# Kernel tuning notes

Hardware: AMD Instinct MI355X
Metric: run time of the kernel (lower is better)

## Reference

```python
import jax, jax.numpy as jnp
import numpy as np

N_INPUT = 2
N_NODES = 4
C = 64          # channel width of every state
B, H, W = 64, 32, 32
N_EDGES = sum(N_INPUT + i for i in range(N_NODES))  # 2+3+4+5 = 14


def conv1x1(x, w):
    # x: [B,C,H,W], w: [C_out,C_in] -> [B,C_out,H,W]
    return jnp.einsum('bchw,oc->bohw', x, w)


def setup_inputs() -> dict:
    key = jax.random.key(0)
    k0, k1, k2, k3 = jax.random.split(key, 4)
    x0 = jax.random.normal(k0, (B, C, H, W), dtype=jnp.float32)
    x1 = jax.random.normal(k1, (B, C, H, W), dtype=jnp.float32)
    # preproc: one 1x1 conv per input state
    W_pre = jax.random.normal(k2, (N_INPUT, C, C), dtype=jnp.float32) * (1.0 / np.sqrt(C))
    # one 1x1 conv per DAG edge (flattened in enumeration order)
    W_edge = jax.random.normal(k3, (N_EDGES, C, C), dtype=jnp.float32) * (1.0 / np.sqrt(C))
    return {'x0': x0, 'x1': x1, 'W_pre': W_pre, 'W_edge': W_edge}


def reference(x0, x1, W_pre, W_edge):
    # preprocess inputs -> initial states
    states = [conv1x1(x0, W_pre[0]), conv1x1(x1, W_pre[1])]
    e = 0
    for i in range(N_NODES):
        n_states = N_INPUT + i
        # gather every prior state, apply edge op (ReLU -> 1x1 conv), sum-merge
        s_cur = conv1x1(jax.nn.relu(states[0]), W_edge[e])
        for s in range(1, n_states):
            s_cur = s_cur + conv1x1(jax.nn.relu(states[s]), W_edge[e + s])
        e += n_states
        states.append(s_cur)
    # merger_out: concat intermediate node states (start=n_input) on channels
    return jnp.concatenate(states[N_INPUT:], axis=1)  # [B, N_NODES*C, H, W]
```

## Files before the change

### kernel.cpp

```cpp
#include <hip/hip_runtime.h>


typedef _Float16 f16;
typedef _Float16 f16x8 __attribute__((ext_vector_type(8)));
typedef float    f32x4 __attribute__((ext_vector_type(4)));

#define RSH 72
#define SB  (64 * RSH)

__device__ __forceinline__ unsigned int pkrtz(float a, float b) {
    __fp16 h2 __attribute__((ext_vector_type(2))) = __builtin_amdgcn_cvt_pkrtz(a, b);
    return __builtin_bit_cast(unsigned int, h2);
}

__global__ __launch_bounds__(256) void wconv_kernel(
    const float* __restrict__ Wpre, const float* __restrict__ Wedge,
    f16* __restrict__ ws)
{
    const int u   = blockIdx.x * 256 + threadIdx.x;
    const int k   = u >> 9;
    const int rem = u & 511;
    const int g   = rem >> 6;
    const int row = rem & 63;
    const float* src = ((k < 2) ? (Wpre + k * 4096) : (Wedge + (k - 2) * 4096))
                       + row * 64 + (g >> 2) * 32 + (g & 3) * 8;
    float4 v0 = ((const float4*)src)[0];
    float4 v1 = ((const float4*)src)[1];
    ((uint4*)ws)[u] = make_uint4(pkrtz(v0.x, v0.y), pkrtz(v0.z, v0.w),
                                 pkrtz(v1.x, v1.y), pkrtz(v1.z, v1.w));
}

__global__ __launch_bounds__(128, 2) void dag_kernel(
    const float* __restrict__ x0, const float* __restrict__ x1,
    const f16* __restrict__ wf, float* __restrict__ out)
{
    __shared__ __align__(16) f16 lds[4 * SB];

    const int t    = threadIdx.x;
    const int lane = t & 63;
    const int wv   = t >> 6;
    const int pl   = lane & 15;
    const int q    = lane >> 4;

    const int blk = blockIdx.x;
    const int b   = blk >> 4;
    const int hw0 = (blk & 15) * 64;

    const float* xg[2] = { x0 + b * 65536 + hw0, x1 + b * 65536 + hw0 };
    float* outg = out + b * 262144 + hw0;

    const f16* wl = wf + q * 512 + pl * 8;

    f16x8 wA[2][2][4];
    #pragma unroll
    for (int kb = 0; kb < 2; ++kb)
        #pragma unroll
        for (int i = 0; i < 4; ++i)
            wA[0][kb][i] = *(const f16x8*)(wl + kb * 2048 + i * 128);

    {
        const int p = t & 63, h = t >> 6;
        #pragma unroll
        for (int inp = 0; inp < 2; ++inp) {
            const float* src = xg[inp] + (h * 32) * 1024 + p;
            unsigned int u[16];
            #pragma unroll
            for (int i = 0; i < 16; ++i)
                u[i] = pkrtz(src[(2 * i) * 1024], src[(2 * i + 1) * 1024]);
            uint4* dst = (uint4*)(lds + (2 + inp) * SB + p * RSH + h * 32);
            dst[0] = make_uint4(u[0],  u[1],  u[2],  u[3]);
            dst[1] = make_uint4(u[4],  u[5],  u[6],  u[7]);
            dst[2] = make_uint4(u[8],  u[9],  u[10], u[11]);
            dst[3] = make_uint4(u[12], u[13], u[14], u[15]);
        }
    }
    __syncthreads();

    f32x4 accA[2][4] = {};
    f32x4 accB[2][4] = {};

    const int widx_tab[16] = {0,1, 2,3, 4,5,6, 7,11, 8,12, 9,13, 14, 10, 15};
    const int src_tab [16] = {2,3, 0,1, 0,1,2, 0,0,  1,1,  2,2,  3,  3,  0};
    const int asel_tab[16] = {0,0, 0,0, 0,0,0, 0,1,  0,1,  0,1,  1,  0,  1};
    const int out_tab [16] = {-1,-1, -1,0, -1,-1,1, -1,-1, -1,-1, -1,-1, -1, 2, 3};
    const int dst_tab [16] = { 0, 1, -1,2, -1,-1,3, -1,-1, -1,-1, -1,-1, -1, 0,-1};

    #pragma unroll
    for (int k = 0; k < 16; ++k) {
        const int cur = k & 1, nxt = cur ^ 1;

        if (k < 15) {
            const f16* wn = wl + widx_tab[k + 1] * 4096;
            #pragma unroll
            for (int kb = 0; kb < 2; ++kb)
                #pragma unroll
                for (int i = 0; i < 4; ++i)
                    wA[nxt][kb][i] = *(const f16x8*)(wn + kb * 2048 + i * 128);
        }

        const f16* S = lds + src_tab[k] * SB;
        f16x8 bf[2][2];
        #pragma unroll
        for (int jj = 0; jj < 2; ++jj)
            #pragma unroll
            for (int kb = 0; kb < 2; ++kb)
                bf[jj][kb] = *(const f16x8*)(S + (wv * 32 + jj * 16 + pl) * RSH
                                               + kb * 32 + q * 8);

        auto step = [&](f32x4 (&acc)[2][4]) {
            #pragma unroll
            for (int jj = 0; jj < 2; ++jj)
                #pragma unroll
                for (int kb = 0; kb < 2; ++kb)
                    #pragma unroll
                    for (int i = 0; i < 4; ++i)
                        acc[jj][i] = __builtin_amdgcn_mfma_f32_16x16x32_f16(
                                         wA[cur][kb][i], bf[jj][kb], acc[jj][i], 0, 0, 0);
        };
        auto retire = [&](f32x4 (&acc)[2][4]) {
            if (out_tab[k] >= 0) {
                #pragma unroll
                for (int jj = 0; jj < 2; ++jj) {
                    const int p = wv * 32 + jj * 16 + pl;
                    #pragma unroll
                    for (int i = 0; i < 4; ++i) {
                        const int c = i * 16 + q * 4;
                        #pragma unroll
                        for (int r = 0; r < 4; ++r)
                            outg[(out_tab[k] * 64 + c + r) * 1024 + p] = acc[jj][i][r];
                    }
                }
            }
            if (dst_tab[k] >= 0) {
                f16* D = lds + dst_tab[k] * SB;
                #pragma unroll
                for (int jj = 0; jj < 2; ++jj) {
                    f16* Dp = D + (wv * 32 + jj * 16 + pl) * RSH;
                    #pragma unroll
                    for (int i = 0; i < 4; ++i) {
                        unsigned int u0 = pkrtz(fmaxf(acc[jj][i][0], 0.f),
                                                fmaxf(acc[jj][i][1], 0.f));
                        unsigned int u1 = pkrtz(fmaxf(acc[jj][i][2], 0.f),
                                                fmaxf(acc[jj][i][3], 0.f));
                        *(uint2*)(Dp + i * 16 + q * 4) = make_uint2(u0, u1);
                    }
                }
            }
            if (out_tab[k] >= 0 || dst_tab[k] >= 0) {
                #pragma unroll
                for (int jj = 0; jj < 2; ++jj)
                    #pragma unroll
                    for (int i = 0; i < 4; ++i)
                        acc[jj][i] = (f32x4){0.f, 0.f, 0.f, 0.f};
            }
        };

        if (asel_tab[k] == 0) { step(accA); retire(accA); }
        else                  { step(accB); retire(accB); }
    }
}

extern "C" void kernel_launch(void* const* d_in, const int* in_sizes, int n_in,
                              void* d_out, int out_size, void* d_ws, size_t ws_size,
                              hipStream_t stream) {
    const float* x0    = (const float*)d_in[0];
    const float* x1    = (const float*)d_in[1];
    const float* Wpre  = (const float*)d_in[2];
    const float* Wedge = (const float*)d_in[3];
    float* outp        = (float*)d_out;
    f16*   wfrag       = (f16*)d_ws;

    wconv_kernel<<<dim3(32), dim3(256), 0, stream>>>(Wpre, Wedge, wfrag);
    dag_kernel<<<dim3(1024), dim3(128), 0, stream>>>(x0, x1, wfrag, outp);
}
```

Before: 104.3 us.

## Swap MFMA operands for DAG edges to vectorize output stores; triple-buffer weights

```diff
diff --git a/kernel.cpp b/kernel.cpp
--- a/kernel.cpp
+++ b/kernel.cpp
@@ -49,14 +49,23 @@
     const float* xg[2] = { x0 + b * 65536 + hw0, x1 + b * 65536 + hw0 };
     float* outg = out + b * 262144 + hw0;
 
+    const int widx_tab[16] = {0,1, 2,3, 4,5,6, 7,11, 8,12, 9,13, 14, 10, 15};
+    const int src_tab [16] = {2,3, 0,1, 0,1,2, 0,0,  1,1,  2,2,  3,  3,  0};
+    const int asel_tab[16] = {0,0, 0,0, 0,0,0, 0,1,  0,1,  0,1,  1,  0,  1};
+    const int out_tab [16] = {-1,-1, -1,0, -1,-1,1, -1,-1, -1,-1, -1,-1, -1, 2, 3};
+    const int dst_tab [16] = { 0, 1, -1,2, -1,-1,3, -1,-1, -1,-1, -1,-1, -1, 0,-1};
+
     const f16* wl = wf + q * 512 + pl * 8;
 
-    f16x8 wA[2][2][4];
+    f16x8 wA[3][2][4];
     #pragma unroll
-    for (int kb = 0; kb < 2; ++kb)
+    for (int s = 0; s < 2; ++s)
         #pragma unroll
-        for (int i = 0; i < 4; ++i)
-            wA[0][kb][i] = *(const f16x8*)(wl + kb * 2048 + i * 128);
+        for (int kb = 0; kb < 2; ++kb)
+            #pragma unroll
+            for (int i = 0; i < 4; ++i)
+                wA[s][kb][i] = *(const f16x8*)(wl + widx_tab[s] * 4096
+                                               + kb * 2048 + i * 128);
 
     {
         const int p = t & 63, h = t >> 6;
@@ -79,23 +88,18 @@
     f32x4 accA[2][4] = {};
     f32x4 accB[2][4] = {};
 
-    const int widx_tab[16] = {0,1, 2,3, 4,5,6, 7,11, 8,12, 9,13, 14, 10, 15};
-    const int src_tab [16] = {2,3, 0,1, 0,1,2, 0,0,  1,1,  2,2,  3,  3,  0};
-    const int asel_tab[16] = {0,0, 0,0, 0,0,0, 0,1,  0,1,  0,1,  1,  0,  1};
-    const int out_tab [16] = {-1,-1, -1,0, -1,-1,1, -1,-1, -1,-1, -1,-1, -1, 2, 3};
-    const int dst_tab [16] = { 0, 1, -1,2, -1,-1,3, -1,-1, -1,-1, -1,-1, -1, 0,-1};
-
     #pragma unroll
     for (int k = 0; k < 16; ++k) {
-        const int cur = k & 1, nxt = cur ^ 1;
+        const int cur = k % 3;
 
-        if (k < 15) {
-            const f16* wn = wl + widx_tab[k + 1] * 4096;
+        if (k < 14) {
+            const f16* wn = wl + widx_tab[k + 2] * 4096;
+            const int s = (k + 2) % 3;
             #pragma unroll
             for (int kb = 0; kb < 2; ++kb)
                 #pragma unroll
                 for (int i = 0; i < 4; ++i)
-                    wA[nxt][kb][i] = *(const f16x8*)(wn + kb * 2048 + i * 128);
+                    wA[s][kb][i] = *(const f16x8*)(wn + kb * 2048 + i * 128);
         }
 
         const f16* S = lds + src_tab[k] * SB;
@@ -107,6 +111,8 @@
                 bf[jj][kb] = *(const f16x8*)(S + (wv * 32 + jj * 16 + pl) * RSH
                                                + kb * 32 + q * 8);
 
+        const bool swp = (k >= 2);
+
         auto step = [&](f32x4 (&acc)[2][4]) {
             #pragma unroll
             for (int jj = 0; jj < 2; ++jj)
@@ -114,35 +120,48 @@
                 for (int kb = 0; kb < 2; ++kb)
                     #pragma unroll
                     for (int i = 0; i < 4; ++i)
-                        acc[jj][i] = __builtin_amdgcn_mfma_f32_16x16x32_f16(
-                                         wA[cur][kb][i], bf[jj][kb], acc[jj][i], 0, 0, 0);
+                        acc[jj][i] = swp
+                            ? __builtin_amdgcn_mfma_f32_16x16x32_f16(
+                                  bf[jj][kb], wA[cur][kb][i], acc[jj][i], 0, 0, 0)
+                            : __builtin_amdgcn_mfma_f32_16x16x32_f16(
+                                  wA[cur][kb][i], bf[jj][kb], acc[jj][i], 0, 0, 0);
         };
         auto retire = [&](f32x4 (&acc)[2][4]) {
             if (out_tab[k] >= 0) {
                 #pragma unroll
                 for (int jj = 0; jj < 2; ++jj) {
-                    const int p = wv * 32 + jj * 16 + pl;
+                    const int p0 = wv * 32 + jj * 16 + q * 4;
                     #pragma unroll
-                    for (int i = 0; i < 4; ++i) {
-                        const int c = i * 16 + q * 4;
-                        #pragma unroll
-                        for (int r = 0; r < 4; ++r)
-                            outg[(out_tab[k] * 64 + c + r) * 1024 + p] = acc[jj][i][r];
-                    }
+                    for (int i = 0; i < 4; ++i)
+                        *(f32x4*)(outg + (out_tab[k] * 64 + i * 16 + pl) * 1024
+                                       + p0) = acc[jj][i];
                 }
             }
             if (dst_tab[k] >= 0) {
                 f16* D = lds + dst_tab[k] * SB;
-                #pragma unroll
-                for (int jj = 0; jj < 2; ++jj) {
-                    f16* Dp = D + (wv * 32 + jj * 16 + pl) * RSH;
+                if (!swp) {
                     #pragma unroll
-                    for (int i = 0; i < 4; ++i) {
-                        unsigned int u0 = pkrtz(fmaxf(acc[jj][i][0], 0.f),
-                                                fmaxf(acc[jj][i][1], 0.f));
-                        unsigned int u1 = pkrtz(fmaxf(acc[jj][i][2], 0.f),
-                                                fmaxf(acc[jj][i][3], 0.f));
-                        *(uint2*)(Dp + i * 16 + q * 4) = make_uint2(u0, u1);
+                    for (int jj = 0; jj < 2; ++jj) {
+                        f16* Dp = D + (wv * 32 + jj * 16 + pl) * RSH;
+                        #pragma unroll
+                        for (int i = 0; i < 4; ++i) {
+                            unsigned int u0 = pkrtz(fmaxf(acc[jj][i][0], 0.f),
+                                                    fmaxf(acc[jj][i][1], 0.f));
+                            unsigned int u1 = pkrtz(fmaxf(acc[jj][i][2], 0.f),
+                                                    fmaxf(acc[jj][i][3], 0.f));
+                            *(uint2*)(Dp + i * 16 + q * 4) = make_uint2(u0, u1);
+                        }
+                    }
+                } else {
+                    #pragma unroll
+                    for (int jj = 0; jj < 2; ++jj) {
+                        const int p0 = wv * 32 + jj * 16 + q * 4;
+                        #pragma unroll
+                        for (int i = 0; i < 4; ++i)
+                            #pragma unroll
+                            for (int r = 0; r < 4; ++r)
+                                D[(p0 + r) * RSH + i * 16 + pl] =
+                                    (f16)fmaxf(acc[jj][i][r], 0.f);
                     }
                 }
             }
```

Result: slower. 107.2 us (+2.8%).

## Split output channels across four waves and swap MFMA operands for vectorized stores

Applied to the files above, without the earlier changes.

```diff
diff --git a/kernel.cpp b/kernel.cpp
--- a/kernel.cpp
+++ b/kernel.cpp
@@ -30,7 +30,7 @@
                                  pkrtz(v1.x, v1.y), pkrtz(v1.z, v1.w));
 }
 
-__global__ __launch_bounds__(128, 2) void dag_kernel(
+__global__ __launch_bounds__(256, 4) void dag_kernel(
     const float* __restrict__ x0, const float* __restrict__ x1,
     const f16* __restrict__ wf, float* __restrict__ out)
 {
@@ -38,7 +38,7 @@
 
     const int t    = threadIdx.x;
     const int lane = t & 63;
-    const int wv   = t >> 6;
+    const int w    = t >> 6;
     const int pl   = lane & 15;
     const int q    = lane >> 4;
 
@@ -49,41 +49,37 @@
     const float* xg[2] = { x0 + b * 65536 + hw0, x1 + b * 65536 + hw0 };
     float* outg = out + b * 262144 + hw0;
 
-    const f16* wl = wf + q * 512 + pl * 8;
+    const f16* wl = wf + q * 512 + (w * 16 + pl) * 8;
 
-    f16x8 wA[2][2][4];
+    f16x8 wA[2][2];
     #pragma unroll
     for (int kb = 0; kb < 2; ++kb)
-        #pragma unroll
-        for (int i = 0; i < 4; ++i)
-            wA[0][kb][i] = *(const f16x8*)(wl + kb * 2048 + i * 128);
+        wA[0][kb] = *(const f16x8*)(wl + kb * 2048);
 
     {
         const int p = t & 63, h = t >> 6;
         #pragma unroll
         for (int inp = 0; inp < 2; ++inp) {
-            const float* src = xg[inp] + (h * 32) * 1024 + p;
-            unsigned int u[16];
+            const float* src = xg[inp] + (h * 16) * 1024 + p;
+            unsigned int u[8];
             #pragma unroll
-            for (int i = 0; i < 16; ++i)
+            for (int i = 0; i < 8; ++i)
                 u[i] = pkrtz(src[(2 * i) * 1024], src[(2 * i + 1) * 1024]);
-            uint4* dst = (uint4*)(lds + (2 + inp) * SB + p * RSH + h * 32);
-            dst[0] = make_uint4(u[0],  u[1],  u[2],  u[3]);
-            dst[1] = make_uint4(u[4],  u[5],  u[6],  u[7]);
-            dst[2] = make_uint4(u[8],  u[9],  u[10], u[11]);
-            dst[3] = make_uint4(u[12], u[13], u[14], u[15]);
+            uint4* dst = (uint4*)(lds + (2 + inp) * SB + p * RSH + h * 16);
+            dst[0] = make_uint4(u[0], u[1], u[2], u[3]);
+            dst[1] = make_uint4(u[4], u[5], u[6], u[7]);
         }
     }
     __syncthreads();
 
-    f32x4 accA[2][4] = {};
-    f32x4 accB[2][4] = {};
+    f32x4 accA[4] = {};
+    f32x4 accB[4] = {};
 
-    const int widx_tab[16] = {0,1, 2,3, 4,5,6, 7,11, 8,12, 9,13, 14, 10, 15};
-    const int src_tab [16] = {2,3, 0,1, 0,1,2, 0,0,  1,1,  2,2,  3,  3,  0};
-    const int asel_tab[16] = {0,0, 0,0, 0,0,0, 0,1,  0,1,  0,1,  1,  0,  1};
-    const int out_tab [16] = {-1,-1, -1,0, -1,-1,1, -1,-1, -1,-1, -1,-1, -1, 2, 3};
-    const int dst_tab [16] = { 0, 1, -1,2, -1,-1,3, -1,-1, -1,-1, -1,-1, -1, 0,-1};
+    const int widx_tab[16] = {0,1, 2,11, 3, 4,12, 5,13, 6, 7, 8, 9,10, 14,15};
+    const int src_tab [16] = {2,3, 0, 0, 1, 0, 1, 1, 2, 2, 0, 1, 2, 3,  3, 0};
+    const int asel_tab[16] = {0,0, 0, 1, 0, 0, 1, 0, 1, 0, 0, 0, 0, 0,  1, 1};
+    const int out_tab [16] = {-1,-1,-1,-1, 0,-1,-1,-1,-1, 1,-1,-1,-1, 2,-1, 3};
+    const int dst_tab [16] = { 0, 1,-1,-1, 2,-1,-1,-1,-1, 3,-1,-1,-1, 0,-1,-1};
 
     #pragma unroll
     for (int k = 0; k < 16; ++k) {
@@ -93,66 +89,66 @@
             const f16* wn = wl + widx_tab[k + 1] * 4096;
             #pragma unroll
             for (int kb = 0; kb < 2; ++kb)
-                #pragma unroll
-                for (int i = 0; i < 4; ++i)
-                    wA[nxt][kb][i] = *(const f16x8*)(wn + kb * 2048 + i * 128);
+                wA[nxt][kb] = *(const f16x8*)(wn + kb * 2048);
         }
 
         const f16* S = lds + src_tab[k] * SB;
-        f16x8 bf[2][2];
+        f16x8 bf[4][2];
         #pragma unroll
-        for (int jj = 0; jj < 2; ++jj)
+        for (int jj = 0; jj < 4; ++jj)
             #pragma unroll
             for (int kb = 0; kb < 2; ++kb)
-                bf[jj][kb] = *(const f16x8*)(S + (wv * 32 + jj * 16 + pl) * RSH
+                bf[jj][kb] = *(const f16x8*)(S + (jj * 16 + pl) * RSH
                                                + kb * 32 + q * 8);
 
-        auto step = [&](f32x4 (&acc)[2][4]) {
+        const bool swp = (k >= 2);
+
+        auto step = [&](f32x4 (&acc)[4]) {
             #pragma unroll
-            for (int jj = 0; jj < 2; ++jj)
+            for (int jj = 0; jj < 4; ++jj)
                 #pragma unroll
                 for (int kb = 0; kb < 2; ++kb)
-                    #pragma unroll
-                    for (int i = 0; i < 4; ++i)
-                        acc[jj][i] = __builtin_amdgcn_mfma_f32_16x16x32_f16(
-                                         wA[cur][kb][i], bf[jj][kb], acc[jj][i], 0, 0, 0);
+                    acc[jj] = swp
+                        ? __builtin_amdgcn_mfma_f32_16x16x32_f16(
+                              bf[jj][kb], wA[cur][kb], acc[jj], 0, 0, 0)
+                        : __builtin_amdgcn_mfma_f32_16x16x32_f16(
+                              wA[cur][kb], bf[jj][kb], acc[jj], 0, 0, 0);
         };
-        auto retire = [&](f32x4 (&acc)[2][4]) {
+        auto retire = [&](f32x4 (&acc)[4]) {
+            if (k == 13) __syncthreads();
             if (out_tab[k] >= 0) {
                 #pragma unroll
-                for (int jj = 0; jj < 2; ++jj) {
-                    const int p = wv * 32 + jj * 16 + pl;
-                    #pragma unroll
-                    for (int i = 0; i < 4; ++i) {
-                        const int c = i * 16 + q * 4;
-                        #pragma unroll
-                        for (int r = 0; r < 4; ++r)
-                            outg[(out_tab[k] * 64 + c + r) * 1024 + p] = acc[jj][i][r];
-                    }
-                }
+                for (int jj = 0; jj < 4; ++jj)
+                    *(f32x4*)(outg + (out_tab[k] * 64 + w * 16 + pl) * 1024
+                                   + jj * 16 + q * 4) = acc[jj];
             }
             if (dst_tab[k] >= 0) {
                 f16* D = lds + dst_tab[k] * SB;
-                #pragma unroll
-                for (int jj = 0; jj < 2; ++jj) {
-                    f16* Dp = D + (wv * 32 + jj * 16 + pl) * RSH;
+                if (!swp) {
                     #pragma unroll
-                    for (int i = 0; i < 4; ++i) {
-                        unsigned int u0 = pkrtz(fmaxf(acc[jj][i][0], 0.f),
-                                                fmaxf(acc[jj][i][1], 0.f));
-                        unsigned int u1 = pkrtz(fmaxf(acc[jj][i][2], 0.f),
-                                                fmaxf(acc[jj][i][3], 0.f));
-                        *(uint2*)(Dp + i * 16 + q * 4) = make_uint2(u0, u1);
+                    for (int jj = 0; jj < 4; ++jj) {
+                        unsigned int u0 = pkrtz(fmaxf(acc[jj][0], 0.f),
+                                                fmaxf(acc[jj][1], 0.f));
+                        unsigned int u1 = pkrtz(fmaxf(acc[jj][2], 0.f),
+                                                fmaxf(acc[jj][3], 0.f));
+                        *(uint2*)(D + (jj * 16 + pl) * RSH + w * 16 + q * 4) =
+                            make_uint2(u0, u1);
                     }
+                } else {
+                    #pragma unroll
+                    for (int jj = 0; jj < 4; ++jj)
+                        #pragma unroll
+                        for (int r = 0; r < 4; ++r)
+                            D[(jj * 16 + q * 4 + r) * RSH + w * 16 + pl] =
+                                (f16)fmaxf(acc[jj][r], 0.f);
                 }
             }
             if (out_tab[k] >= 0 || dst_tab[k] >= 0) {
                 #pragma unroll
-                for (int jj = 0; jj < 2; ++jj)
-                    #pragma unroll
-                    for (int i = 0; i < 4; ++i)
-                        acc[jj][i] = (f32x4){0.f, 0.f, 0.f, 0.f};
+                for (int jj = 0; jj < 4; ++jj)
+                    acc[jj] = (f32x4){0.f, 0.f, 0.f, 0.f};
             }
+            if (dst_tab[k] >= 0) __syncthreads();
         };
 
         if (asel_tab[k] == 0) { step(accA); retire(accA); }
@@ -171,5 +167,5 @@
     f16*   wfrag       = (f16*)d_ws;
 
     wconv_kernel<<<dim3(32), dim3(256), 0, stream>>>(Wpre, Wedge, wfrag);
-    dag_kernel<<<dim3(1024), dim3(128), 0, stream>>>(x0, x1, wfrag, outp);
+    dag_kernel<<<dim3(1024), dim3(256), 0, stream>>>(x0, x1, wfrag, outp);
 }
```

Measured after the change: 103.6 us. Within noise of the previous version (-0.7%).
